# Kernel optimization log

Measured on AMD Instinct MI355X. Metric: run time of the kernel, lower is better.

The kernel has to match this reference:

```python
import jax, jax.numpy as jnp
import numpy as np

MUL = 32           # multiplicity of each irrep in Rs_in / Rs_out
R_EPS = 0.1        # radius below which the linear fallback kernel is used
SQRT3 = np.float32(np.sqrt(3.0))

# real-basis Levi-Civita = wigner_3j(1,1,1) * sqrt(6)
_EPS3 = np.zeros((3, 3, 3), np.float32)
_EPS3[0, 1, 2] = _EPS3[1, 2, 0] = _EPS3[2, 0, 1] = 1.0
_EPS3[0, 2, 1] = _EPS3[2, 1, 0] = _EPS3[1, 0, 2] = -1.0


def _frozen_kernel(r, W1, b1, W2, b2, lin_w0, lin_w1):
    N = r.shape[0]
    radii = jnp.linalg.norm(r, axis=1)                 # [N]
    mask = radii > R_EPS                               # [N] valid edges
    safe = jnp.where(mask, radii, jnp.ones_like(radii))
    unit = r / safe[:, None]                           # [N,3] safe unit vectors

    # radial MLP R: r -> R^(5*MUL*MUL); computed densely, masked rows replaced below
    h = jax.nn.relu(radii[:, None] * W1 + b1)          # [N,H]
    R = (h @ W2 + b2).reshape(N, 5, MUL, MUL)          # [N, path, w(out), u(in)]
    R0a, R0b, R1a, R1b, R1c = (R[:, i] for i in range(5))

    # component-normalized spherical harmonics: Y0 = 1, Y1 = sqrt(3)*unit
    Y1 = SQRT3 * unit                                  # [N,3]

    # per-path normalization: 1/sqrt(n_paths_into_output * mul_in)
    n0 = np.float32(1.0 / np.sqrt(2 * MUL))            # output l=0: 2 paths
    n1 = np.float32(1.0 / np.sqrt(3 * MUL))            # output l=1: 3 paths
    I3 = jnp.eye(3, dtype=r.dtype)
    eps3 = jnp.asarray(_EPS3, dtype=r.dtype)

    # CG tensor-product kernel blocks (w3j contracted analytically for l<=1)
    K00 = n0 * R0a                                                      # [N,w,u]
    K01 = (n0 / SQRT3) * jnp.einsum('nwu,ni->nwui', R1b, Y1)            # in l=1 -> out l=0
    K10 = n1 * jnp.einsum('nwu,nj->nwju', R1a, Y1)                      # in l=0 -> out l=1
    K11 = n1 * (jnp.einsum('nwu,ji->nwjui', R0b, I3)                    # l_f=0 path
                + np.float32(1.0 / np.sqrt(2.0))
                * jnp.einsum('nwu,nk,ikj->nwjui', R1c, Y1, eps3))       # l_f=1 path

    D = 4 * MUL  # dim = MUL*(1) + MUL*(3)
    kernel1 = jnp.zeros((N, D, D), r.dtype)
    kernel1 = kernel1.at[:, :MUL, :MUL].set(K00)
    kernel1 = kernel1.at[:, :MUL, MUL:].set(K01.reshape(N, MUL, 3 * MUL))
    kernel1 = kernel1.at[:, MUL:, :MUL].set(K10.reshape(N, 3 * MUL, MUL))
    kernel1 = kernel1.at[:, MUL:, MUL:].set(K11.reshape(N, 3 * MUL, 3 * MUL))

    # KernelLinear fallback for radii <= r_eps: block diag per l, scaled 1/sqrt(mul_in)
    s = np.float32(1.0 / np.sqrt(MUL))
    k2_11 = s * jnp.einsum('wu,ji->wjui', lin_w1, I3).reshape(3 * MUL, 3 * MUL)
    kernel2 = jnp.zeros((D, D), r.dtype)
    kernel2 = kernel2.at[:MUL, :MUL].set(s * lin_w0)
    kernel2 = kernel2.at[MUL:, MUL:].set(k2_11)

    return jnp.where(mask[:, None, None], kernel1, kernel2[None, :, :])


def setup_inputs() -> dict:
    key = jax.random.key(0)
    ks = jax.random.split(key, 6)
    N, H = 4000, 128
    r = jax.random.normal(ks[0], (N, 3), jnp.float32)
    r = r.at[:100].multiply(0.01)  # push some radii under r_eps -> fallback path
    W1 = jax.random.normal(ks[1], (1, H), jnp.float32)
    b1 = jnp.zeros((H,), jnp.float32)
    W2 = jax.random.normal(ks[2], (H, 5 * MUL * MUL), jnp.float32) / np.float32(np.sqrt(H))
    b2 = jnp.zeros((5 * MUL * MUL,), jnp.float32)
    lin_w0 = jax.random.normal(ks[3], (MUL, MUL), jnp.float32)
    lin_w1 = jax.random.normal(ks[4], (MUL, MUL), jnp.float32)
    return dict(r=r, W1=W1, b1=b1, W2=W2, b2=b2, lin_w0=lin_w0, lin_w1=lin_w1)


def reference(r, W1, b1, W2, b2, lin_w0, lin_w1):
    return _frozen_kernel(r, W1, b1, W2, b2, lin_w0, lin_w1)
```

## Files before the change

kernel.cpp:

```cpp
#include <hip/hip_runtime.h>
#include <math.h>

#define H 128
#define MUL 32
#define NC (5 * MUL * MUL)
#define NIV (H + 1)
#define NMAX 4000
#define EPB 4
#define TILE4 4096

typedef float f32x4 __attribute__((ext_vector_type(4)));

__device__ float g_A[NIV * NC];
__device__ float g_B[NIV * NC];
__device__ float4 g_ey[NMAX];
__device__ int    g_eidx[NMAX];

__global__ __launch_bounds__(256) void prep_all(const float* __restrict__ W1,
                                                const float* __restrict__ b1,
                                                const float* __restrict__ W2,
                                                const float* __restrict__ b2,
                                                const float* __restrict__ r, int N) {
    __shared__ float bp[H];
    __shared__ float sorted[H];
    int tid = threadIdx.x;
    bool valid = false;
    float v = 3.0e38f;
    if (tid < H) {
        float a = W1[tid], b = b1[tid];
        if (a != 0.0f) {
            float t = -b / a;
            if (t > 0.0f) { v = t; valid = true; }
        }
        bp[tid] = v;
    }
    int nbp = __syncthreads_count(valid);
    int y = blockIdx.y;
    bool isEdge = (y == NIV);
    if (!isEdge && y > nbp) return;

    if (nbp > 0) {
        if (tid < H) {
            int rank = 0;
            #pragma unroll 8
            for (int j = 0; j < H; ++j) {
                float bj = bp[j];
                rank += (bj < v) || (bj == v && j < tid);
            }
            sorted[rank] = v;
        }
        __syncthreads();
    }

    if (isEdge) {
        int e = blockIdx.x * 256 + tid;
        if (e >= N) return;
        float x = r[3 * e], yy = r[3 * e + 1], z = r[3 * e + 2];
        float rad = sqrtf(x * x + yy * yy + z * z);
        bool mask = rad > 0.1f;
        float inv = mask ? (1.7320508075688772f / rad) : 0.0f;
        g_ey[e] = make_float4(x * inv, yy * inv, z * inv, rad);
        int idx = -1;
        if (mask) {
            idx = 0;
            for (int j = 0; j < nbp; ++j) idx += (sorted[j] < rad) ? 1 : 0;
        }
        g_eidx[e] = idx;
        return;
    }

    float rm;
    if (nbp == 0)       rm = 1.0f;
    else if (y == 0)    rm = 0.5f * sorted[0];
    else if (y >= nbp)  rm = sorted[nbp - 1] + 1.0f;
    else                rm = 0.5f * (sorted[y - 1] + sorted[y]);

    int c = blockIdx.x * 256 + tid;
    float accA = 0.0f, accB = 0.0f;
    #pragma unroll 4
    for (int k = 0; k < H; ++k) {
        float a = W1[k], b = b1[k];
        float w2 = W2[k * NC + c];
        bool act = (a * rm + b) > 0.0f;
        accA += act ? a * w2 : 0.0f;
        accB += act ? b * w2 : 0.0f;
    }
    int p = c >> 10;
    const float n0 = 0.125f;
    const float n1 = 0.10206207261596575f;
    const float ns = 0.07216878364870323f;
    float s = (p == 0) ? n0 : ((p <= 2) ? n1 : ns);
    g_A[y * NC + c] = s * accA;
    g_B[y * NC + c] = s * (accB + b2[c]);
}

__global__ __launch_bounds__(256) void main_kernel(const float* __restrict__ lin_w0,
                                                   const float* __restrict__ lin_w1,
                                                   float* __restrict__ out, int N) {
    int pos  = blockIdx.x * 256 + threadIdx.x;
    int row  = pos >> 5;
    int col0 = (pos & 31) << 2;

    const float s = 0.17677669529663687f;
    int   cidx[4]; int iY[4]; float sgn[4]; float fb[4];

    #pragma unroll
    for (int q = 0; q < 4; ++q) {
        int col = col0 + q;
        int ci, sel; float sg = 1.0f, f = 0.0f;
        if (row < MUL) {
            if (col < MUL) {
                ci = row * MUL + col; sel = 3; f = s * lin_w0[row * MUL + col];
            } else {
                int cc = col - MUL; int u = (cc * 171) >> 9; int i = cc - 3 * u;
                ci = 3 * 1024 + row * MUL + u; sel = i;
            }
        } else {
            int rr = row - MUL; int w = (rr * 171) >> 9; int j = rr - 3 * w;
            if (col < MUL) {
                ci = 2 * 1024 + w * MUL + col; sel = j;
            } else {
                int cc = col - MUL; int u = (cc * 171) >> 9; int i = cc - 3 * u;
                if (i == j) {
                    ci = 1 * 1024 + w * MUL + u; sel = 3; f = s * lin_w1[w * MUL + u];
                } else {
                    int jp = (j == 2) ? 0 : (j + 1);
                    ci = 4 * 1024 + w * MUL + u; sel = 3 - i - j;
                    sg = (i == jp) ? 1.0f : -1.0f;
                }
            }
        }
        cidx[q] = ci; iY[q] = sel; sgn[q] = sg; fb[q] = f;
    }

    int n0 = blockIdx.y * EPB;

    float4 eys[EPB]; int idxs[EPB];
    #pragma unroll
    for (int k = 0; k < EPB; ++k) {
        int n = n0 + k; if (n > N - 1) n = N - 1;
        eys[k] = g_ey[n];
        idxs[k] = g_eidx[n];
    }

    f32x4* base = reinterpret_cast<f32x4*>(out) + (size_t)n0 * TILE4 + pos;
    int cached = -2;
    float Ac[4], Bc[4];

    #pragma unroll
    for (int k = 0; k < EPB; ++k) {
        if (n0 + k >= N) break;
        int idx = idxs[k];
        float4 ey = eys[k];
        f32x4 v;
        if (idx >= 0) {
            if (idx != cached) {
                const float* __restrict__ Ab = g_A + (size_t)idx * NC;
                const float* __restrict__ Bb = g_B + (size_t)idx * NC;
                #pragma unroll
                for (int q = 0; q < 4; ++q) {
                    Ac[q] = sgn[q] * Ab[cidx[q]];
                    Bc[q] = sgn[q] * Bb[cidx[q]];
                }
                cached = idx;
            }
            float rad = ey.w;
            #pragma unroll
            for (int q = 0; q < 4; ++q) {
                float ys = (iY[q] == 0) ? ey.x : ((iY[q] == 1) ? ey.y
                         : ((iY[q] == 2) ? ey.z : 1.0f));
                v[q] = fmaf(rad, Ac[q], Bc[q]) * ys;
            }
        } else {
            #pragma unroll
            for (int q = 0; q < 4; ++q) v[q] = fb[q];
        }
        __builtin_nontemporal_store(v, base + (size_t)k * TILE4);
    }
}

extern "C" void kernel_launch(void* const* d_in, const int* in_sizes, int n_in,
                              void* d_out, int out_size, void* d_ws, size_t ws_size,
                              hipStream_t stream) {
    const float* r   = (const float*)d_in[0];
    const float* W1  = (const float*)d_in[1];
    const float* b1  = (const float*)d_in[2];
    const float* W2  = (const float*)d_in[3];
    const float* b2  = (const float*)d_in[4];
    const float* lw0 = (const float*)d_in[5];
    const float* lw1 = (const float*)d_in[6];
    float* out = (float*)d_out;
    int N = in_sizes[0] / 3;

    prep_all<<<dim3(NC / 256, NIV + 1), dim3(256), 0, stream>>>(W1, b1, W2, b2, r, N);
    int eChunks = (N + EPB - 1) / EPB;
    main_kernel<<<dim3(16, eChunks), dim3(256), 0, stream>>>(lw0, lw1, out, N);
}
```

Before: 61.31 us.

## Convert main kernel to persistent grid-stride loop with edge-data prefetch

Replaces the 2D grid of 4-edge chunks with a fixed grid of 1024 blocks that stride over the flattened output. Each thread keeps its fixed column mapping, since the stride is a multiple of the tile size, and prefetches the next edge's unit vector and interval index before the current iteration's store. This removes per-block setup cost repeated across about 16k blocks. In exchange, per-thread coefficient caching now sees edges 64 apart instead of adjacent ones, so cache hits are less likely.

```diff
diff --git a/kernel.cpp b/kernel.cpp
--- a/kernel.cpp
+++ b/kernel.cpp
@@ -6,8 +6,8 @@
 #define NC (5 * MUL * MUL)
 #define NIV (H + 1)
 #define NMAX 4000
-#define EPB 4
 #define TILE4 4096
+#define MBLK 1024
 
 typedef float f32x4 __attribute__((ext_vector_type(4)));
 
@@ -97,12 +97,13 @@
 __global__ __launch_bounds__(256) void main_kernel(const float* __restrict__ lin_w0,
                                                    const float* __restrict__ lin_w1,
                                                    float* __restrict__ out, int N) {
-    int pos  = blockIdx.x * 256 + threadIdx.x;
+    size_t g0 = (size_t)blockIdx.x * 256 + threadIdx.x;
+    int pos  = (int)(g0 & (TILE4 - 1));
     int row  = pos >> 5;
     int col0 = (pos & 31) << 2;
 
     const float s = 0.17677669529663687f;
-    int   cidx[4]; int iY[4]; float sgn[4]; float fb[4];
+    int cidx[4]; int iY[4]; float sgn[4]; float fb[4];
 
     #pragma unroll
     for (int q = 0; q < 4; ++q) {
@@ -133,25 +134,25 @@
         cidx[q] = ci; iY[q] = sel; sgn[q] = sg; fb[q] = f;
     }
 
-    int n0 = blockIdx.y * EPB;
+    const size_t stride_t = (size_t)MBLK * 256;
+    const int    n_step   = (int)(stride_t >> 12);
+    const size_t total    = (size_t)N * TILE4;
+    f32x4* o = reinterpret_cast<f32x4*>(out);
 
-    float4 eys[EPB]; int idxs[EPB];
-    #pragma unroll
-    for (int k = 0; k < EPB; ++k) {
-        int n = n0 + k; if (n > N - 1) n = N - 1;
-        eys[k] = g_ey[n];
-        idxs[k] = g_eidx[n];
-    }
+    int n = (int)(g0 >> 12);
+    int nc0 = (n < N) ? n : (N - 1);
+    float4 ey = g_ey[nc0];
+    int    idx = g_eidx[nc0];
 
-    f32x4* base = reinterpret_cast<f32x4*>(out) + (size_t)n0 * TILE4 + pos;
     int cached = -2;
     float Ac[4], Bc[4];
 
-    #pragma unroll
-    for (int k = 0; k < EPB; ++k) {
-        if (n0 + k >= N) break;
-        int idx = idxs[k];
-        float4 ey = eys[k];
+    for (size_t g = g0; g < total; g += stride_t) {
+        int np = n + n_step;
+        int npc = (np < N) ? np : (N - 1);
+        float4 ey_nx = g_ey[npc];
+        int    idx_nx = g_eidx[npc];
+
         f32x4 v;
         if (idx >= 0) {
             if (idx != cached) {
@@ -175,7 +176,8 @@
             #pragma unroll
             for (int q = 0; q < 4; ++q) v[q] = fb[q];
         }
-        __builtin_nontemporal_store(v, base + (size_t)k * TILE4);
+        __builtin_nontemporal_store(v, o + g);
+        ey = ey_nx; idx = idx_nx; n = np;
     }
 }
 
@@ -193,6 +195,5 @@
     int N = in_sizes[0] / 3;
 
     prep_all<<<dim3(NC / 256, NIV + 1), dim3(256), 0, stream>>>(W1, b1, W2, b2, r, N);
-    int eChunks = (N + EPB - 1) / EPB;
-    main_kernel<<<dim3(16, eChunks), dim3(256), 0, stream>>>(lw0, lw1, out, N);
+    main_kernel<<<dim3(MBLK), dim3(256), 0, stream>>>(lw0, lw1, out, N);
 }
```

Result: slower. 66.92 us (+9.1%).
